# Optimization experiments

Hardware: AMD Instinct MI355X
Metric: run time of the kernel (lower is better)

## Reference

```python
import jax, jax.numpy as jnp
import numpy as np

B, NQ, NK = 4, 2048, 2048
CQ, CK = 1024, 768
H = 16
D = CQ // H  # 64
EPS = 1e-5


def layernorm(x, gamma, beta):
    mu = jnp.mean(x, axis=-1, keepdims=True)
    var = jnp.var(x, axis=-1, keepdims=True)
    return (x - mu) * jax.lax.rsqrt(var + EPS) * gamma + beta


def setup_inputs() -> dict:
    key = jax.random.key(0)
    ks = jax.random.split(key, 12)
    s_q = 1.0 / np.sqrt(CQ)
    s_c = 1.0 / np.sqrt(CK)
    return {
        "query_tokens": jax.random.normal(ks[0], (B, NQ, CQ), jnp.float32),
        "context_tokens": jax.random.normal(ks[1], (B, NK, CK), jnp.float32),
        "Wq": jax.random.uniform(ks[2], (CQ, CQ), jnp.float32, -s_q, s_q),
        "bq": jnp.zeros((CQ,), jnp.float32),
        "Wk": jax.random.uniform(ks[3], (CK, CQ), jnp.float32, -s_c, s_c),
        "bk": jnp.zeros((CQ,), jnp.float32),
        "Wv": jax.random.uniform(ks[4], (CK, CQ), jnp.float32, -s_c, s_c),
        "bv": jnp.zeros((CQ,), jnp.float32),
        "Wo": jax.random.uniform(ks[5], (CQ, CQ), jnp.float32, -s_q, s_q),
        "bo": jnp.zeros((CQ,), jnp.float32),
        "gamma_q": jnp.ones((CQ,), jnp.float32),
        "beta_q": jnp.zeros((CQ,), jnp.float32),
        "gamma_ctx": jnp.ones((CK,), jnp.float32),
        "beta_ctx": jnp.zeros((CK,), jnp.float32),
    }


def reference(query_tokens, context_tokens, Wq, bq, Wk, bk, Wv, bv, Wo, bo,
              gamma_q, beta_q, gamma_ctx, beta_ctx):
    scale = 1.0 / np.sqrt(D)
    xq = layernorm(query_tokens, gamma_q, beta_q)      # [B,NQ,CQ]
    xc = layernorm(context_tokens, gamma_ctx, beta_ctx)  # [B,NK,CK]
    q = (xq @ Wq + bq).reshape(B, NQ, H, D)
    k = (xc @ Wk + bk).reshape(B, NK, H, D)
    v = (xc @ Wv + bv).reshape(B, NK, H, D)
    scores = jnp.einsum('bqhd,bkhd->bhqk', q, k) * scale  # [B,H,NQ,NK]
    attn = jax.nn.softmax(scores, axis=-1)
    attended = jnp.einsum('bhqk,bkhd->bqhd', attn, v).reshape(B, NQ, CQ)
    return attended @ Wo + bo
```

## Files before the change

kernel.cpp:

```cpp
#include <hip/hip_runtime.h>
#include <hip/hip_bf16.h>
#include <stdint.h>

#define B_    4
#define NQ_   2048
#define NK_   2048
#define CQ_   1024
#define CK_   768
#define H_    16
#define D_    64
#define SCALE 0.125f
#define C2    0.1803368801111204f

typedef __attribute__((ext_vector_type(8))) short bf16x8;
typedef __attribute__((ext_vector_type(4))) float f32x4;
typedef __attribute__((ext_vector_type(4))) unsigned int u32x4;

#define MFMA16(a, b, c) __builtin_amdgcn_mfma_f32_16x16x32_bf16((a), (b), (c), 0, 0, 0)

#define GLL16(gp, lp)                                                                 \
    __builtin_amdgcn_global_load_lds(                                                 \
        (__attribute__((address_space(1))) uint32_t*)(uintptr_t)(gp),                 \
        (__attribute__((address_space(3))) uint32_t*)(uintptr_t)(lp), 16, 0, 0)

__device__ inline unsigned short f2bf(float f) {
    union { float f; uint32_t u; } v; v.f = f;
    uint32_t u = v.u;
    return (unsigned short)((u + 0x7fffu + ((u >> 16) & 1u)) >> 16);
}

__device__ inline uint32_t packbf2(float a, float b) {
    union { __hip_bfloat162 h; uint32_t u; } v;
    v.h = __float22bfloat162_rn(float2{a, b});
    return v.u;
}

__global__ __launch_bounds__(256) void ln_tr(const float* __restrict__ xqt,
                                             const float* __restrict__ xct,
                                             const float* __restrict__ gq,
                                             const float* __restrict__ btq,
                                             const float* __restrict__ gc,
                                             const float* __restrict__ btc,
                                             unsigned short* __restrict__ oq,
                                             unsigned short* __restrict__ oc,
                                             const float* __restrict__ Wq,
                                             const float* __restrict__ Wk,
                                             const float* __restrict__ Wv,
                                             const float* __restrict__ Wo,
                                             unsigned short* __restrict__ Wqt,
                                             unsigned short* __restrict__ Wkvt,
                                             unsigned short* __restrict__ Wot) {
    __shared__ float red[8];
    __shared__ float stat[2];
    __shared__ float tt[32][33];
    int blk = blockIdx.x;
    int tid = threadIdx.x;

    if (blk < 16384) {
        const float *x, *gamma, *beta;
        unsigned short* out;
        int W;
        float invW;
        if (blk < 8192) {
            x = xqt + (size_t)blk * 1024; gamma = gq; beta = btq;
            out = oq + (size_t)blk * 1024; W = 1024; invW = 1.f / 1024.f;
        } else {
            int r = blk - 8192;
            x = xct + (size_t)r * 768; gamma = gc; beta = btc;
            out = oc + (size_t)r * 768; W = 768; invW = 1.f / 768.f;
        }
        int col = tid * 4;
        float v0 = 0.f, v1 = 0.f, v2 = 0.f, v3 = 0.f;
        float s = 0.f, s2 = 0.f;
        bool active = (col < W);
        if (active) {
            float4 vv = *(const float4*)(x + col);
            v0 = vv.x; v1 = vv.y; v2 = vv.z; v3 = vv.w;
            s = v0 + v1 + v2 + v3;
            s2 = v0 * v0 + v1 * v1 + v2 * v2 + v3 * v3;
        }
        for (int off = 32; off >= 1; off >>= 1) {
            s += __shfl_xor(s, off);
            s2 += __shfl_xor(s2, off);
        }
        int wid = tid >> 6, lane = tid & 63;
        if (lane == 0) { red[wid] = s; red[4 + wid] = s2; }
        __syncthreads();
        if (tid == 0) {
            float ts = red[0] + red[1] + red[2] + red[3];
            float ts2 = red[4] + red[5] + red[6] + red[7];
            float mu = ts * invW;
            float var = ts2 * invW - mu * mu;
            stat[0] = mu;
            stat[1] = rsqrtf(var + 1e-5f);
        }
        __syncthreads();
        float mu = stat[0], rstd = stat[1];
        if (active) {
            float4 gm = *(const float4*)(gamma + col);
            float4 bt = *(const float4*)(beta + col);
            ushort4 o;
            o.x = f2bf((v0 - mu) * rstd * gm.x + bt.x);
            o.y = f2bf((v1 - mu) * rstd * gm.y + bt.y);
            o.z = f2bf((v2 - mu) * rstd * gm.z + bt.z);
            o.w = f2bf((v3 - mu) * rstd * gm.w + bt.w);
            *(ushort4*)(out + col) = o;
        }
    } else {
        int b2 = blk - 16384;
        const float* src;
        unsigned short* dst;
        int K;
        if (b2 < 1024)      { src = Wq; dst = Wqt; K = 1024; }
        else if (b2 < 1792) { b2 -= 1024; src = Wk; dst = Wkvt; K = 768; }
        else if (b2 < 2560) { b2 -= 1792; src = Wv; dst = Wkvt + (size_t)1024 * 768; K = 768; }
        else                 { b2 -= 2560; src = Wo; dst = Wot; K = 1024; }
        int n0 = (b2 & 31) * 32, k0 = (b2 >> 5) * 32;
        int tx = tid & 31, ty = tid >> 5;
        for (int i = 0; i < 4; i++)
            tt[ty + 8 * i][tx] = src[(size_t)(k0 + ty + 8 * i) * 1024 + n0 + tx];
        __syncthreads();
        for (int i = 0; i < 4; i++)
            dst[(size_t)(n0 + ty + 8 * i) * K + k0 + tx] = f2bf(tt[tx][ty + 8 * i]);
    }
}

__global__ __launch_bounds__(512) void gemm_qkv(const unsigned short* __restrict__ xq,
                                                const unsigned short* __restrict__ Wqt,
                                                const float* __restrict__ bq,
                                                const unsigned short* __restrict__ xc,
                                                const unsigned short* __restrict__ Wkvt,
                                                const float* __restrict__ bk,
                                                const float* __restrict__ bv,
                                                unsigned short* __restrict__ Qb,
                                                unsigned short* __restrict__ Kb,
                                                unsigned short* __restrict__ Vtb) {
    __shared__ __align__(16) unsigned short As[128 * 64];
    __shared__ __align__(16) unsigned short Bs[256 * 64];
    int tid = threadIdx.x;
    int lane = tid & 63, wid = tid >> 6;
    int q = lane & 15, g = lane >> 4;

    int lin = blockIdx.x;
    int xcd = lin & 7;
    int idx = lin >> 3;
    const unsigned short *X, *Wt;
    int Kd, NB, sub, qrole;
    if (idx < 32) { X = xq; Wt = Wqt;  Kd = 1024; NB = 4; sub = xcd * 32 + idx;         qrole = 1; }
    else          { X = xc; Wt = Wkvt; Kd = 768;  NB = 8; sub = xcd * 64 + (idx - 32);  qrole = 0; }
    int m0 = (sub / NB) * 128;
    int n0 = (sub % NB) * 256;
    int wm = wid >> 2, wn = wid & 3;

    f32x4 acc[4][4];
    for (int i = 0; i < 4; i++)
        for (int j = 0; j < 4; j++) acc[i][j] = (f32x4){0.f, 0.f, 0.f, 0.f};

    int srow = wid * 8 + (lane >> 3);
    int sxor = ((lane & 7) * 16) ^ (((lane >> 3) & 7) << 4);
    int swz = (lane & 7) << 4;
    const char* Xb = (const char*)X;
    const char* Wb = (const char*)Wt;
    char* AsB = (char*)As;
    char* BsB = (char*)Bs;

    for (int k0 = 0; k0 < Kd; k0 += 64) {
#pragma unroll
        for (int i = 0; i < 2; i++) {
            int row = i * 64 + srow;
            GLL16(Xb + ((size_t)(m0 + row) * Kd + k0) * 2 + sxor, AsB + i * 8192 + wid * 1024);
        }
#pragma unroll
        for (int i = 0; i < 4; i++) {
            int row = i * 64 + srow;
            GLL16(Wb + ((size_t)(n0 + row) * Kd + k0) * 2 + sxor, BsB + i * 8192 + wid * 1024);
        }
        __syncthreads();
#pragma unroll
        for (int kk = 0; kk < 2; kk++) {
            int cb = ((g * 16 + kk * 64) ^ swz);
            bf16x8 a[4], b[4];
#pragma unroll
            for (int mf = 0; mf < 4; mf++)
                a[mf] = *(const bf16x8*)(AsB + (wm * 64 + mf * 16 + q) * 128 + cb);
#pragma unroll
            for (int nf = 0; nf < 4; nf++)
                b[nf] = *(const bf16x8*)(BsB + (wn * 64 + nf * 16 + q) * 128 + cb);
#pragma unroll
            for (int mf = 0; mf < 4; mf++)
#pragma unroll
                for (int nf = 0; nf < 4; nf++) acc[mf][nf] = MFMA16(a[mf], b[nf], acc[mf][nf]);
        }
        __syncthreads();
    }

    int crow0 = m0 + wm * 64;
    int ccol0 = n0 + wn * 64;
    for (int nf = 0; nf < 4; nf++) {
        int col = ccol0 + nf * 16 + q;
        float bv_ = qrole ? bq[col] : ((col < 1024) ? bk[col] : bv[col - 1024]);
        if (!qrole && col >= 1024) {
            int c = col - 1024;
            int h = c >> 6, d = c & 63;
            for (int mf = 0; mf < 4; mf++) {
                int rowb = crow0 + mf * 16 + g * 4;
                int b = rowb >> 11;
                int nqb = rowb & 2047;
                int u = nqb & 63;
                int pbase = (nqb & ~63) | ((u & 32) + ((u & 12) << 1) + ((u & 16) >> 2));
                ushort4 o;
                o.x = f2bf(acc[mf][nf][0] + bv_);
                o.y = f2bf(acc[mf][nf][1] + bv_);
                o.z = f2bf(acc[mf][nf][2] + bv_);
                o.w = f2bf(acc[mf][nf][3] + bv_);
                *(ushort4*)&Vtb[(((size_t)(b * H_ + h)) * 64 + d) * NK_ + pbase] = o;
            }
        } else {
            for (int mf = 0; mf < 4; mf++) {
                int rowb = crow0 + mf * 16 + g * 4;
                for (int r = 0; r < 4; r++) {
                    int row = rowb + r;
                    float val = acc[mf][nf][r] + bv_;
                    int b = row >> 11, nq = row & 2047;
                    int h = col >> 6, d = col & 63;
                    if (qrole) {
                        Qb[(((size_t)(b * H_ + h)) * NQ_ + nq) * 64 + d] = f2bf(val * C2);
                    } else {
                        Kb[(((size_t)(b * H_ + h)) * NQ_ + nq) * 64 + d] = f2bf(val);
                    }
                }
            }
        }
    }
}

__global__ __launch_bounds__(256) void gemm_out(const unsigned short* __restrict__ X,
                                                const unsigned short* __restrict__ Wt,
                                                const float* __restrict__ bias0,
                                                float* __restrict__ out0) {
    __shared__ __align__(16) unsigned short As[4][128 * 32];
    __shared__ __align__(16) unsigned short Bs[4][128 * 32];
    int tid = threadIdx.x;
    int lane = tid & 63, wid = tid >> 6;
    int q = lane & 15, g = lane >> 4;
    const int Kd = 1024;

    int lin = blockIdx.y * 8 + blockIdx.x;
    int virt = (lin & 7) * 64 + (lin >> 3);
    int m0 = (virt / 8) * 128;
    int n0 = (virt % 8) * 128;
    int wm = wid >> 1, wn = wid & 1;

    f32x4 acc[4][4];
    for (int i = 0; i < 4; i++)
        for (int j = 0; j < 4; j++) acc[i][j] = (f32x4){0.f, 0.f, 0.f, 0.f};

    int sx2 = (((lane & 3) ^ ((lane >> 2) & 3)) << 4);
    int srow0 = wid * 32 + (lane >> 2);
    const char* Xb = (const char*)X;
    const char* Wb = (const char*)Wt;
    char* AsB = (char*)As;
    char* BsB = (char*)Bs;

    auto STAGE = [&](int buf, int t) {
#pragma unroll
        for (int c = 0; c < 2; c++) {
            int row = srow0 + c * 16;
            GLL16(Xb + ((size_t)(m0 + row) * Kd + t * 32) * 2 + sx2,
                  AsB + buf * 8192 + wid * 2048 + c * 1024);
            GLL16(Wb + ((size_t)(n0 + row) * Kd + t * 32) * 2 + sx2,
                  BsB + buf * 8192 + wid * 2048 + c * 1024);
        }
    };

    int ck = (g ^ (q & 3)) << 4;
    auto COMPUTE = [&](int buf) {
        bf16x8 a[4], b[4];
#pragma unroll
        for (int mf = 0; mf < 4; mf++)
            a[mf] = *(const bf16x8*)(AsB + buf * 8192 + (wm * 64 + mf * 16 + q) * 64 + ck);
#pragma unroll
        for (int nf = 0; nf < 4; nf++)
            b[nf] = *(const bf16x8*)(BsB + buf * 8192 + (wn * 64 + nf * 16 + q) * 64 + ck);
#pragma unroll
        for (int mf = 0; mf < 4; mf++)
#pragma unroll
            for (int nf = 0; nf < 4; nf++) acc[mf][nf] = MFMA16(a[mf], b[nf], acc[mf][nf]);
    };

    const int nT = 32;
    STAGE(0, 0);
    STAGE(1, 1);
    STAGE(2, 2);
    STAGE(3, 3);
    __syncthreads();

    for (int i = 0; i < nT / 2; i++) {
        int t = 2 * i;
        COMPUTE(t & 3);
        COMPUTE((t + 1) & 3);
        __syncthreads();
        if (t + 4 < nT) {
            STAGE(t & 3, t + 4);
            STAGE((t + 1) & 3, t + 5);
        }
    }

    int crow0 = m0 + wm * 64;
    int ccol0 = n0 + wn * 64;
    for (int nf = 0; nf < 4; nf++) {
        int col = ccol0 + nf * 16 + q;
        float bv_ = bias0[col];
        for (int mf = 0; mf < 4; mf++) {
            int rowb = crow0 + mf * 16 + g * 4;
            for (int r = 0; r < 4; r++) {
                int row = rowb + r;
                out0[(size_t)row * 1024 + col] = acc[mf][nf][r] + bv_;
            }
        }
    }
}

__global__ __launch_bounds__(512, 4) void flash_attn(const unsigned short* __restrict__ Q,
                                                     const unsigned short* __restrict__ K,
                                                     const unsigned short* __restrict__ Vt,
                                                     unsigned short* __restrict__ attended) {
    __shared__ __align__(16) char smem[4][16384];
    int tid = threadIdx.x, lane = tid & 63, wid = tid >> 6;
    int g = lane >> 4;
    int q = lane & 15;

    const f32x4 zero4 = {0.f, 0.f, 0.f, 0.f};

    int lin = blockIdx.y * 8 + blockIdx.x;
    int virt = (lin & 7) * 64 + (lin >> 3);
    int bh = virt >> 3;
    int q0 = (virt & 7) * 256;
    const char* Qb = (const char*)(Q + (size_t)bh * NQ_ * 64);
    const char* Kb = (const char*)(K + (size_t)bh * NK_ * 64);
    const char* Vb = (const char*)(Vt + (size_t)bh * 64 * NK_);

    int qrow = q0 + wid * 32 + q;
    bf16x8 qf0[2], qf1[2];
    qf0[0] = *(const bf16x8*)(Qb + (size_t)qrow * 128 + g * 16);
    qf0[1] = *(const bf16x8*)(Qb + (size_t)qrow * 128 + g * 16 + 64);
    qf1[0] = *(const bf16x8*)(Qb + (size_t)(qrow + 16) * 128 + g * 16);
    qf1[1] = *(const bf16x8*)(Qb + (size_t)(qrow + 16) * 128 + g * 16 + 64);

    bf16x8 onesf;
#pragma unroll
    for (int i = 0; i < 8; i++) onesf[i] = (short)0x3f80;

    f32x4 acc0[4], acc1[4];
    for (int i = 0; i < 4; i++) {
        acc0[i] = zero4;
        acc1[i] = zero4;
    }
    f32x4 accl0 = zero4, accl1 = zero4;

    int sxor = ((lane & 7) * 16) ^ (((lane >> 3) & 7) << 4);
    const char* kptr = Kb + (size_t)(wid * 8 + (lane >> 3)) * 128 + sxor;
    const char* vptr = Vb + (size_t)(wid * 8 + (lane >> 3)) * 4096 + sxor;
    int cb0 = g * 16;
    int swz = (lane & 7) << 4;

    auto TILE = [&](const char* Ksb, const char* Vsb) {
        f32x4 s0[4], s1[4];
        __builtin_amdgcn_s_setprio(1);
#pragma unroll
        for (int nf = 0; nf < 4; nf++) {
            bf16x8 kf0 = *(const bf16x8*)(Ksb + (nf * 16 + q) * 128 + (cb0 ^ swz));
            bf16x8 kf1 = *(const bf16x8*)(Ksb + (nf * 16 + q) * 128 + ((cb0 + 64) ^ swz));
            s0[nf] = MFMA16(kf0, qf0[0], zero4);
            s0[nf] = MFMA16(kf1, qf0[1], s0[nf]);
            s1[nf] = MFMA16(kf0, qf1[0], zero4);
            s1[nf] = MFMA16(kf1, qf1[1], s1[nf]);
        }
        __builtin_amdgcn_s_setprio(0);

        __builtin_amdgcn_s_setprio(1);
#pragma unroll
        for (int kk = 0; kk < 2; kk++) {
            float p0v[8], p1v[8];
#pragma unroll
            for (int h = 0; h < 2; h++)
#pragma unroll
                for (int r = 0; r < 4; r++) {
                    p0v[4 * h + r] = __builtin_amdgcn_exp2f(s0[2 * kk + h][r]);
                    p1v[4 * h + r] = __builtin_amdgcn_exp2f(s1[2 * kk + h][r]);
                }
            union { u32x4 u; bf16x8 b; } ap0, ap1;
            ap0.u[0] = packbf2(p0v[0], p0v[1]);
            ap0.u[1] = packbf2(p0v[2], p0v[3]);
            ap0.u[2] = packbf2(p0v[4], p0v[5]);
            ap0.u[3] = packbf2(p0v[6], p0v[7]);
            ap1.u[0] = packbf2(p1v[0], p1v[1]);
            ap1.u[1] = packbf2(p1v[2], p1v[3]);
            ap1.u[2] = packbf2(p1v[4], p1v[5]);
            ap1.u[3] = packbf2(p1v[6], p1v[7]);

            accl0 = MFMA16(ap0.b, onesf, accl0);
            accl1 = MFMA16(ap1.b, onesf, accl1);
#pragma unroll
            for (int df = 0; df < 4; df++) {
                bf16x8 bv = *(const bf16x8*)(Vsb + (df * 16 + q) * 128 + ((cb0 + kk * 64) ^ swz));
                acc0[df] = MFMA16(ap0.b, bv, acc0[df]);
                acc1[df] = MFMA16(ap1.b, bv, acc1[df]);
            }
        }
        __builtin_amdgcn_s_setprio(0);
    };

#pragma unroll
    for (int j = 0; j < 4; j++) {
        GLL16(kptr, smem[j] + wid * 1024);
        GLL16(vptr, smem[j] + 8192 + wid * 1024);
        kptr += 8192;
        vptr += 128;
    }
    __syncthreads();

    for (int i = 0; i < 16; ++i) {
        int t = 2 * i;
        const char* B0 = smem[t & 3];
        const char* B1 = smem[(t + 1) & 3];
        TILE(B0, B0 + 8192);
        TILE(B1, B1 + 8192);
        __syncthreads();
        if (t + 4 < 32) {
            GLL16(kptr, smem[t & 3] + wid * 1024);
            GLL16(vptr, smem[t & 3] + 8192 + wid * 1024);
            kptr += 8192;
            vptr += 128;
            GLL16(kptr, smem[(t + 1) & 3] + wid * 1024);
            GLL16(vptr, smem[(t + 1) & 3] + 8192 + wid * 1024);
            kptr += 8192;
            vptr += 128;
        }
    }

    int b = bh >> 4, h = bh & 15;
#pragma unroll
    for (int df = 0; df < 4; df++)
#pragma unroll
        for (int r = 0; r < 4; r++) {
            int row = q0 + wid * 32 + 4 * g + r;
            int col = h * 64 + df * 16 + q;
            attended[(size_t)(b * NQ_ + row) * CQ_ + col] = f2bf(acc0[df][r] / accl0[r]);
            attended[(size_t)(b * NQ_ + row + 16) * CQ_ + col] = f2bf(acc1[df][r] / accl1[r]);
        }
}

extern "C" void kernel_launch(void* const* d_in, const int* in_sizes, int n_in,
                              void* d_out, int out_size, void* d_ws, size_t ws_size,
                              hipStream_t stream) {
    const float* qt  = (const float*)d_in[0];
    const float* ct  = (const float*)d_in[1];
    const float* Wq  = (const float*)d_in[2];
    const float* bq  = (const float*)d_in[3];
    const float* Wk  = (const float*)d_in[4];
    const float* bk  = (const float*)d_in[5];
    const float* Wv  = (const float*)d_in[6];
    const float* bv  = (const float*)d_in[7];
    const float* Wo  = (const float*)d_in[8];
    const float* bo  = (const float*)d_in[9];
    const float* gq  = (const float*)d_in[10];
    const float* btq = (const float*)d_in[11];
    const float* gc  = (const float*)d_in[12];
    const float* btc = (const float*)d_in[13];

    char* ws = (char*)d_ws;
    unsigned short* xq   = (unsigned short*)(ws + 0);
    unsigned short* xc   = (unsigned short*)(ws + 16777216);
    unsigned short* Wqt  = (unsigned short*)(ws + 29360128);
    unsigned short* Wkvt = (unsigned short*)(ws + 31457280);
    unsigned short* Wot  = (unsigned short*)(ws + 34603008);
    unsigned short* Qb   = (unsigned short*)(ws + 36700160);
    unsigned short* Kb   = (unsigned short*)(ws + 53477376);
    unsigned short* Vtb  = (unsigned short*)(ws + 70254592);

    ln_tr<<<19968, 256, 0, stream>>>(qt, ct, gq, btq, gc, btc, xq, xc,
                                     Wq, Wk, Wv, Wo, Wqt, Wkvt, Wot);

    gemm_qkv<<<768, 512, 0, stream>>>(xq, Wqt, bq, xc, Wkvt, bk, bv, Qb, Kb, Vtb);

    flash_attn<<<dim3(8, 64), 512, 0, stream>>>(Qb, Kb, Vtb, xq);

    gemm_out<<<dim3(8, 64), 256, 0, stream>>>(xq, Wot, bo, (float*)d_out);
}
```

Before: 169.1 us.

## Retile output GEMM to 128x256 tiles with 512 threads, single-buffered K=64 steps

Output projection GEMM moves from 128x128 tiles on 256 threads with a 4-deep K=32 LDS pipeline to 128x256 tiles on 512 threads with single-buffered K=64 steps and a new XOR swizzle. Block-to-XCD mapping is redone for 256 blocks. The larger tile is meant to raise operand reuse and cut redundant global loads of X. In exchange the prefetch pipelining is dropped, so load latency is no longer overlapped with compute and there are two barriers per K step. With 256 blocks there is also only about one block per CU.

```diff
diff --git a/kernel.cpp b/kernel.cpp
--- a/kernel.cpp
+++ b/kernel.cpp
@@ -234,76 +234,64 @@
     }
 }
 
-__global__ __launch_bounds__(256) void gemm_out(const unsigned short* __restrict__ X,
+__global__ __launch_bounds__(512) void gemm_out(const unsigned short* __restrict__ X,
                                                 const unsigned short* __restrict__ Wt,
                                                 const float* __restrict__ bias0,
                                                 float* __restrict__ out0) {
-    __shared__ __align__(16) unsigned short As[4][128 * 32];
-    __shared__ __align__(16) unsigned short Bs[4][128 * 32];
+    __shared__ __align__(16) unsigned short As[128 * 64];
+    __shared__ __align__(16) unsigned short Bs[256 * 64];
     int tid = threadIdx.x;
     int lane = tid & 63, wid = tid >> 6;
     int q = lane & 15, g = lane >> 4;
     const int Kd = 1024;
 
-    int lin = blockIdx.y * 8 + blockIdx.x;
-    int virt = (lin & 7) * 64 + (lin >> 3);
-    int m0 = (virt / 8) * 128;
-    int n0 = (virt % 8) * 128;
-    int wm = wid >> 1, wn = wid & 1;
+    int lin = blockIdx.x;
+    int xcd = lin & 7;
+    int sub = xcd * 32 + (lin >> 3);
+    int m0 = (sub >> 2) * 128;
+    int n0 = (sub & 3) * 256;
+    int wm = wid >> 2, wn = wid & 3;
 
     f32x4 acc[4][4];
     for (int i = 0; i < 4; i++)
         for (int j = 0; j < 4; j++) acc[i][j] = (f32x4){0.f, 0.f, 0.f, 0.f};
 
-    int sx2 = (((lane & 3) ^ ((lane >> 2) & 3)) << 4);
-    int srow0 = wid * 32 + (lane >> 2);
+    int srow = wid * 8 + (lane >> 3);
+    int sxor = ((lane & 7) * 16) ^ (((lane >> 3) & 7) << 4);
+    int swz = (lane & 7) << 4;
     const char* Xb = (const char*)X;
     const char* Wb = (const char*)Wt;
     char* AsB = (char*)As;
     char* BsB = (char*)Bs;
 
-    auto STAGE = [&](int buf, int t) {
-#pragma unroll
-        for (int c = 0; c < 2; c++) {
-            int row = srow0 + c * 16;
-            GLL16(Xb + ((size_t)(m0 + row) * Kd + t * 32) * 2 + sx2,
-                  AsB + buf * 8192 + wid * 2048 + c * 1024);
-            GLL16(Wb + ((size_t)(n0 + row) * Kd + t * 32) * 2 + sx2,
-                  BsB + buf * 8192 + wid * 2048 + c * 1024);
-        }
-    };
-
-    int ck = (g ^ (q & 3)) << 4;
-    auto COMPUTE = [&](int buf) {
-        bf16x8 a[4], b[4];
-#pragma unroll
-        for (int mf = 0; mf < 4; mf++)
-            a[mf] = *(const bf16x8*)(AsB + buf * 8192 + (wm * 64 + mf * 16 + q) * 64 + ck);
-#pragma unroll
-        for (int nf = 0; nf < 4; nf++)
-            b[nf] = *(const bf16x8*)(BsB + buf * 8192 + (wn * 64 + nf * 16 + q) * 64 + ck);
-#pragma unroll
-        for (int mf = 0; mf < 4; mf++)
-#pragma unroll
-            for (int nf = 0; nf < 4; nf++) acc[mf][nf] = MFMA16(a[mf], b[nf], acc[mf][nf]);
-    };
-
-    const int nT = 32;
-    STAGE(0, 0);
-    STAGE(1, 1);
-    STAGE(2, 2);
-    STAGE(3, 3);
-    __syncthreads();
-
-    for (int i = 0; i < nT / 2; i++) {
-        int t = 2 * i;
-        COMPUTE(t & 3);
-        COMPUTE((t + 1) & 3);
-        __syncthreads();
-        if (t + 4 < nT) {
-            STAGE(t & 3, t + 4);
-            STAGE((t + 1) & 3, t + 5);
-        }
+    for (int k0 = 0; k0 < Kd; k0 += 64) {
+#pragma unroll
+        for (int i = 0; i < 2; i++) {
+            int row = i * 64 + srow;
+            GLL16(Xb + ((size_t)(m0 + row) * Kd + k0) * 2 + sxor, AsB + i * 8192 + wid * 1024);
+        }
+#pragma unroll
+        for (int i = 0; i < 4; i++) {
+            int row = i * 64 + srow;
+            GLL16(Wb + ((size_t)(n0 + row) * Kd + k0) * 2 + sxor, BsB + i * 8192 + wid * 1024);
+        }
+        __syncthreads();
+#pragma unroll
+        for (int kk = 0; kk < 2; kk++) {
+            int cb = ((g * 16 + kk * 64) ^ swz);
+            bf16x8 a[4], b[4];
+#pragma unroll
+            for (int mf = 0; mf < 4; mf++)
+                a[mf] = *(const bf16x8*)(AsB + (wm * 64 + mf * 16 + q) * 128 + cb);
+#pragma unroll
+            for (int nf = 0; nf < 4; nf++)
+                b[nf] = *(const bf16x8*)(BsB + (wn * 64 + nf * 16 + q) * 128 + cb);
+#pragma unroll
+            for (int mf = 0; mf < 4; mf++)
+#pragma unroll
+                for (int nf = 0; nf < 4; nf++) acc[mf][nf] = MFMA16(a[mf], b[nf], acc[mf][nf]);
+        }
+        __syncthreads();
     }
 
     int crow0 = m0 + wm * 64;
@@ -486,5 +474,5 @@
 
     flash_attn<<<dim3(8, 64), 512, 0, stream>>>(Qb, Kb, Vtb, xq);
 
-    gemm_out<<<dim3(8, 64), 256, 0, stream>>>(xq, Wot, bo, (float*)d_out);
-}
+    gemm_out<<<256, 512, 0, stream>>>(xq, Wot, bo, (float*)d_out);
+}
```

After: 173.2 us. 2.5% more time.
